# Performance work log

Hardware: AMD Instinct MI355X
Metric: run time of the kernel (lower is better)

## Reference

```python
import jax, jax.numpy as jnp
import numpy as np

ITERATIONS = 3


def squash(s):
    # Faithful to the torch code: norm is taken over axis 2 (the labels axis
    # for s_j of shape (B, 1, L, O)), exactly as torch's squash(dim=2) does.
    mag_sq = jnp.sum(s * s, axis=2, keepdims=True)
    mag = jnp.sqrt(mag_sq)
    return mag_sq / (1.0 + mag_sq) * (s / mag)


def setup_inputs() -> dict:
    key = jax.random.key(0)
    kx, kw = jax.random.split(key)
    B, N, P, L, O = 256, 8, 1152, 10, 16
    x = jax.random.normal(kx, (B, N, P), dtype=jnp.float32)
    # nn.Parameter(torch.randn(1, P, L, O, N))
    W = jax.random.normal(kw, (1, P, L, O, N), dtype=jnp.float32)
    return {"x": x, "W": W}


def reference(x, W):
    # x: (B, N, P), W: (1, P, L, O, N)
    _, P, L, O, N = W.shape
    u = jnp.transpose(x, (0, 2, 1))  # (B, P, N)
    # u_hat[b,p,l,o] = sum_n W[0,p,l,o,n] * u[b,p,n]
    u_hat = jnp.einsum('plon,bpn->bplo', W[0], u)  # (B, P, L, O)

    b_ij = jnp.zeros((1, P, L, 1), dtype=u_hat.dtype)
    v_j = None
    for _ in range(ITERATIONS):
        # softmax over a size-1 trailing axis -> all ones (faithful to source)
        c_ij = jax.nn.softmax(b_ij, axis=-1)           # (1, P, L, 1)
        s_j = jnp.sum(c_ij * u_hat, axis=1, keepdims=True)  # (B, 1, L, O)
        v_j = squash(s_j)                               # (B, 1, L, O)
        # agreement: <u_hat, v_j> over output dim, then mean over batch
        agree = jnp.einsum('bplo,blo->bpl', u_hat, v_j[:, 0])  # (B, P, L)
        b_ij = b_ij + jnp.mean(agree, axis=0)[None, :, :, None]
    return jnp.squeeze(v_j)  # (B, L, O)
```

## Files before the change

### kernel.cpp

```cpp
#include <hip/hip_runtime.h>
#include <hip/hip_bf16.h>
#include <math.h>

#define B_TOT 256
#define N_N   8
#define P_P   1152
#define J_J   160
#define K_K   9216
#define L_L   10

#define SG 18
#define JG 5

typedef __attribute__((ext_vector_type(8))) short short8;
typedef __attribute__((ext_vector_type(4))) float f32x4;

__device__ __forceinline__ short f2bf(float f) {
    __hip_bfloat16 h = __float2bfloat16(f);
    return __builtin_bit_cast(short, h);
}

__global__ __launch_bounds__(256) void gemm_direct(const float* __restrict__ x,
                                                   const float* __restrict__ W,
                                                   float* __restrict__ part) {
    const int bt = blockIdx.x;
    const int sg = blockIdx.y;
    const int jg = blockIdx.z;
    const int tid  = threadIdx.x;
    const int w    = tid >> 6;
    const int lane = tid & 63;
    const int b0 = bt * 32;
    const int p0 = sg * 64;
    const int j0 = jg * 32;

    __shared__ short As[32][520];
    __shared__ float redux[4][64][17];

    #pragma unroll
    for (int i = 0; i < 8; ++i) {
        const int bb = w * 8 + i;
        const float* xr = x + (size_t)(b0 + bb) * K_K + p0 + lane;
        short8 sh;
        #pragma unroll
        for (int n = 0; n < 8; ++n)
            sh[n] = f2bf(xr[(size_t)n * P_P]);
        *reinterpret_cast<short8*>(&As[bb][lane * 8]) = sh;
    }
    __syncthreads();

    const int m  = lane & 15;
    const int kq = lane >> 4;

    f32x4 acc00 = {0.f, 0.f, 0.f, 0.f};
    f32x4 acc01 = {0.f, 0.f, 0.f, 0.f};
    f32x4 acc10 = {0.f, 0.f, 0.f, 0.f};
    f32x4 acc11 = {0.f, 0.f, 0.f, 0.f};

    const float* wbase = W + (size_t)(p0 + w * 16 + kq) * 1280 + (size_t)(j0 + m) * 8;

    #pragma unroll
    for (int ks = 0; ks < 4; ++ks) {
        const short8 af0 =
            *reinterpret_cast<const short8*>(&As[m][w * 128 + ks * 32 + kq * 8]);
        const short8 af1 =
            *reinterpret_cast<const short8*>(&As[m + 16][w * 128 + ks * 32 + kq * 8]);
        const float* wp0 = wbase + (size_t)ks * 4 * 1280;
        const float* wp1 = wp0 + 128;
        const f32x4 a0 = *reinterpret_cast<const f32x4*>(wp0);
        const f32x4 a1 = *reinterpret_cast<const f32x4*>(wp0 + 4);
        const f32x4 c0 = *reinterpret_cast<const f32x4*>(wp1);
        const f32x4 c1 = *reinterpret_cast<const f32x4*>(wp1 + 4);
        short8 bf0, bf1;
        bf0[0] = f2bf(a0.x); bf0[1] = f2bf(a0.y); bf0[2] = f2bf(a0.z); bf0[3] = f2bf(a0.w);
        bf0[4] = f2bf(a1.x); bf0[5] = f2bf(a1.y); bf0[6] = f2bf(a1.z); bf0[7] = f2bf(a1.w);
        bf1[0] = f2bf(c0.x); bf1[1] = f2bf(c0.y); bf1[2] = f2bf(c0.z); bf1[3] = f2bf(c0.w);
        bf1[4] = f2bf(c1.x); bf1[5] = f2bf(c1.y); bf1[6] = f2bf(c1.z); bf1[7] = f2bf(c1.w);
        acc00 = __builtin_amdgcn_mfma_f32_16x16x32_bf16(af0, bf0, acc00, 0, 0, 0);
        acc01 = __builtin_amdgcn_mfma_f32_16x16x32_bf16(af0, bf1, acc01, 0, 0, 0);
        acc10 = __builtin_amdgcn_mfma_f32_16x16x32_bf16(af1, bf0, acc10, 0, 0, 0);
        acc11 = __builtin_amdgcn_mfma_f32_16x16x32_bf16(af1, bf1, acc11, 0, 0, 0);
    }

    #pragma unroll
    for (int r = 0; r < 4; ++r) {
        redux[w][lane][r]      = acc00[r];
        redux[w][lane][r + 4]  = acc01[r];
        redux[w][lane][r + 8]  = acc10[r];
        redux[w][lane][r + 12] = acc11[r];
    }
    __syncthreads();

    #pragma unroll
    for (int f = tid; f < 1024; f += 256) {
        const int ln = f >> 4;
        const int c  = f & 15;
        const float s = redux[0][ln][c] + redux[1][ln][c]
                      + redux[2][ln][c] + redux[3][ln][c];
        const int mm = ln & 15;
        const int kk = ln >> 4;
        const int bi = c >> 3;
        const int ji = (c >> 2) & 1;
        const int r  = c & 3;
        const int b  = b0 + bi * 16 + kk * 4 + r;
        const int j  = j0 + ji * 16 + mm;
        part[((size_t)b * SG + sg) * J_J + j] = s;
    }
}

__global__ __launch_bounds__(192) void reduce_squash(const float* __restrict__ part,
                                                     float* __restrict__ out) {
    const int b = blockIdx.x;
    const int j = threadIdx.x;
    __shared__ float sld[J_J];
    float s = 0.0f;
    if (j < J_J) {
        const float* pb = part + (size_t)b * SG * J_J + j;
        #pragma unroll 6
        for (int si = 0; si < SG; ++si)
            s += pb[(size_t)si * J_J];
        sld[j] = s;
    }
    __syncthreads();
    if (j < J_J) {
        const int o = j & 15;
        float msq = 0.0f;
        #pragma unroll
        for (int l = 0; l < L_L; ++l) {
            const float v = sld[l * 16 + o];
            msq = fmaf(v, v, msq);
        }
        const float mag = sqrtf(msq);
        out[(size_t)b * J_J + j] = s * (mag / (1.0f + msq));
    }
}

extern "C" void kernel_launch(void* const* d_in, const int* in_sizes, int n_in,
                              void* d_out, int out_size, void* d_ws, size_t ws_size,
                              hipStream_t stream) {
    const float* x = (const float*)d_in[0];
    const float* W = (const float*)d_in[1];
    float* out = (float*)d_out;

    float* part = (float*)d_ws;

    dim3 gg(B_TOT / 32, SG, JG);
    gemm_direct<<<gg, 256, 0, stream>>>(x, W, part);

    reduce_squash<<<B_TOT, 192, 0, stream>>>(part, out);
}
```

Baseline: 18.06 us.

## Batch global loads up front, alias reduction buffer onto LDS tile, coalesce output writes

All x loads and all W fragment loads are issued up front into registers, so their latencies overlap instead of being interleaved with conversion and MFMA work. The reduction scratch now reuses the As shared-memory buffer behind an extra barrier, cutting LDS use, and launch bounds request 4 blocks per SM for more occupancy. The final store loop is remapped so consecutive threads write consecutive j, giving coalesced writes to the partial buffer. Holding the prefetched values raises register pressure, which may conflict with the occupancy hint.

```diff
diff --git a/kernel.cpp b/kernel.cpp
--- a/kernel.cpp
+++ b/kernel.cpp
@@ -3,7 +3,6 @@
 #include <math.h>
 
 #define B_TOT 256
-#define N_N   8
 #define P_P   1152
 #define J_J   160
 #define K_K   9216
@@ -20,9 +19,9 @@
     return __builtin_bit_cast(short, h);
 }
 
-__global__ __launch_bounds__(256) void gemm_direct(const float* __restrict__ x,
-                                                   const float* __restrict__ W,
-                                                   float* __restrict__ part) {
+__global__ __launch_bounds__(256, 4) void gemm_direct(const float* __restrict__ x,
+                                                      const float* __restrict__ W,
+                                                      float* __restrict__ part) {
     const int bt = blockIdx.x;
     const int sg = blockIdx.y;
     const int jg = blockIdx.z;
@@ -33,30 +32,43 @@
     const int p0 = sg * 64;
     const int j0 = jg * 32;
 
-    __shared__ short As[32][520];
-    __shared__ float redux[4][64][17];
+    __shared__ __align__(16) short As[32][520];
+    float (*redux)[64][17] = (float (*)[64][17])(&As[0][0]);
 
+    float xv[8][8];
+    {
+        const float* xb = x + (size_t)(b0 + w * 8) * K_K + p0 + lane;
+        #pragma unroll
+        for (int i = 0; i < 8; ++i)
+            #pragma unroll
+            for (int n = 0; n < 8; ++n)
+                xv[i][n] = xb[(size_t)i * K_K + (size_t)n * P_P];
+    }
     #pragma unroll
     for (int i = 0; i < 8; ++i) {
-        const int bb = w * 8 + i;
-        const float* xr = x + (size_t)(b0 + bb) * K_K + p0 + lane;
         short8 sh;
         #pragma unroll
-        for (int n = 0; n < 8; ++n)
-            sh[n] = f2bf(xr[(size_t)n * P_P]);
-        *reinterpret_cast<short8*>(&As[bb][lane * 8]) = sh;
+        for (int n = 0; n < 8; ++n) sh[n] = f2bf(xv[i][n]);
+        *reinterpret_cast<short8*>(&As[w * 8 + i][lane * 8]) = sh;
     }
     __syncthreads();
 
     const int m  = lane & 15;
     const int kq = lane >> 4;
 
-    f32x4 acc00 = {0.f, 0.f, 0.f, 0.f};
-    f32x4 acc01 = {0.f, 0.f, 0.f, 0.f};
-    f32x4 acc10 = {0.f, 0.f, 0.f, 0.f};
-    f32x4 acc11 = {0.f, 0.f, 0.f, 0.f};
+    const float* wbase = W + (size_t)(p0 + w * 16 + kq) * 1280 + (size_t)(j0 + m) * 8;
+    f32x4 bv[4][4];
+    #pragma unroll
+    for (int ks = 0; ks < 4; ++ks) {
+        const float* wp = wbase + (size_t)ks * 4 * 1280;
+        bv[ks][0] = *reinterpret_cast<const f32x4*>(wp);
+        bv[ks][1] = *reinterpret_cast<const f32x4*>(wp + 4);
+        bv[ks][2] = *reinterpret_cast<const f32x4*>(wp + 128);
+        bv[ks][3] = *reinterpret_cast<const f32x4*>(wp + 132);
+    }
 
-    const float* wbase = W + (size_t)(p0 + w * 16 + kq) * 1280 + (size_t)(j0 + m) * 8;
+    f32x4 acc00 = {0.f,0.f,0.f,0.f}, acc01 = {0.f,0.f,0.f,0.f};
+    f32x4 acc10 = {0.f,0.f,0.f,0.f}, acc11 = {0.f,0.f,0.f,0.f};
 
     #pragma unroll
     for (int ks = 0; ks < 4; ++ks) {
@@ -64,22 +76,21 @@
             *reinterpret_cast<const short8*>(&As[m][w * 128 + ks * 32 + kq * 8]);
         const short8 af1 =
             *reinterpret_cast<const short8*>(&As[m + 16][w * 128 + ks * 32 + kq * 8]);
-        const float* wp0 = wbase + (size_t)ks * 4 * 1280;
-        const float* wp1 = wp0 + 128;
-        const f32x4 a0 = *reinterpret_cast<const f32x4*>(wp0);
-        const f32x4 a1 = *reinterpret_cast<const f32x4*>(wp0 + 4);
-        const f32x4 c0 = *reinterpret_cast<const f32x4*>(wp1);
-        const f32x4 c1 = *reinterpret_cast<const f32x4*>(wp1 + 4);
         short8 bf0, bf1;
-        bf0[0] = f2bf(a0.x); bf0[1] = f2bf(a0.y); bf0[2] = f2bf(a0.z); bf0[3] = f2bf(a0.w);
-        bf0[4] = f2bf(a1.x); bf0[5] = f2bf(a1.y); bf0[6] = f2bf(a1.z); bf0[7] = f2bf(a1.w);
-        bf1[0] = f2bf(c0.x); bf1[1] = f2bf(c0.y); bf1[2] = f2bf(c0.z); bf1[3] = f2bf(c0.w);
-        bf1[4] = f2bf(c1.x); bf1[5] = f2bf(c1.y); bf1[6] = f2bf(c1.z); bf1[7] = f2bf(c1.w);
+        #pragma unroll
+        for (int e = 0; e < 4; ++e) {
+            bf0[e]     = f2bf(bv[ks][0][e]);
+            bf0[e + 4] = f2bf(bv[ks][1][e]);
+            bf1[e]     = f2bf(bv[ks][2][e]);
+            bf1[e + 4] = f2bf(bv[ks][3][e]);
+        }
         acc00 = __builtin_amdgcn_mfma_f32_16x16x32_bf16(af0, bf0, acc00, 0, 0, 0);
         acc01 = __builtin_amdgcn_mfma_f32_16x16x32_bf16(af0, bf1, acc01, 0, 0, 0);
         acc10 = __builtin_amdgcn_mfma_f32_16x16x32_bf16(af1, bf0, acc10, 0, 0, 0);
         acc11 = __builtin_amdgcn_mfma_f32_16x16x32_bf16(af1, bf1, acc11, 0, 0, 0);
     }
+
+    __syncthreads();
 
     #pragma unroll
     for (int r = 0; r < 4; ++r) {
@@ -92,18 +103,18 @@
 
     #pragma unroll
     for (int f = tid; f < 1024; f += 256) {
-        const int ln = f >> 4;
-        const int c  = f & 15;
+        const int bl = f >> 5;
+        const int jl = f & 31;
+        const int bi = bl >> 4;
+        const int kk = (bl >> 2) & 3;
+        const int r  = bl & 3;
+        const int ji = jl >> 4;
+        const int mm = jl & 15;
+        const int ln = kk * 16 + mm;
+        const int c  = bi * 8 + ji * 4 + r;
         const float s = redux[0][ln][c] + redux[1][ln][c]
                       + redux[2][ln][c] + redux[3][ln][c];
-        const int mm = ln & 15;
-        const int kk = ln >> 4;
-        const int bi = c >> 3;
-        const int ji = (c >> 2) & 1;
-        const int r  = c & 3;
-        const int b  = b0 + bi * 16 + kk * 4 + r;
-        const int j  = j0 + ji * 16 + mm;
-        part[((size_t)b * SG + sg) * J_J + j] = s;
+        part[((size_t)(b0 + bl) * SG + sg) * J_J + j0 + jl] = s;
     }
 }
 
```

New measurement: 18.19 us. About the same (+0.7%).
